# Optimization experiments

Hardware: AMD Instinct MI355X
Metric: run time of the kernel (lower is better)

## Reference

```python
import jax, jax.numpy as jnp
import numpy as np
import math

B, N, C_IN = 4, 512, 32
K = 3            # Chebyshev order -> K+1 polynomial terms
H = 4            # attention heads
OUT_PER_HEAD = 64
ACT_OUT = OUT_PER_HEAD * H  # concat_heads=True


def _prelu(x, a):
    return jnp.where(x >= 0, x, a * x)


def setup_inputs() -> dict:
    key = jax.random.key(0)
    ks = jax.random.split(key, 10)
    stdv = 1.0 / math.sqrt(ACT_OUT)
    inp = {
        "X_real": jax.random.normal(ks[0], (B, N, C_IN), jnp.float32),
        "X_imag": jax.random.normal(ks[1], (B, N, C_IN), jnp.float32),
        "L_real": jax.random.normal(ks[2], (B, K + 1, N, N), jnp.float32),
        "L_imag": jax.random.normal(ks[3], (B, K + 1, N, N), jnp.float32),
        # Chebyshev complex weights, uniform(-stdv, stdv) as in torch init
        "weight_real": jax.random.uniform(ks[4], (K + 1, C_IN, ACT_OUT), jnp.float32, -stdv, stdv),
        "weight_imag": jax.random.uniform(ks[5], (K + 1, C_IN, ACT_OUT), jnp.float32, -stdv, stdv),
        # CVLinear(2*C_IN -> H) complex weight/bias
        "attn_w_real": jax.random.normal(ks[6], (2 * C_IN, H), jnp.float32) * 0.1,
        "attn_w_imag": jax.random.normal(ks[7], (2 * C_IN, H), jnp.float32) * 0.1,
        "attn_b_real": jnp.zeros((H,), jnp.float32),
        "attn_b_imag": jnp.zeros((H,), jnp.float32),
        # CPReLU slopes (PReLU applied to real/imag parts independently)
        "prelu_a_real": jnp.float32(0.25),
        "prelu_a_imag": jnp.float32(0.25),
        "bias_real": jnp.zeros((1, ACT_OUT), jnp.float32),
        "bias_imag": jnp.zeros((1, ACT_OUT), jnp.float32),
    }
    return inp


def reference(X_real, X_imag, L_real, L_imag, weight_real, weight_imag,
              attn_w_real, attn_w_imag, attn_b_real, attn_b_imag,
              prelu_a_real, prelu_a_imag, bias_real, bias_imag):
    C = X_real.shape[-1]
    K1 = weight_real.shape[0]
    # --- attention scores: complex linear on concat([X_i, X_j]) ---
    # split the 2C weight into the X_i half and the X_j half (same math,
    # avoids materializing the B*N*N*2C pairwise concat tensor)
    W1r, W2r = attn_w_real[:C], attn_w_real[C:]
    W1i, W2i = attn_w_imag[:C], attn_w_imag[C:]
    si_re = X_real @ W1r - X_imag @ W1i   # (B,N,H)
    si_im = X_real @ W1i + X_imag @ W1r
    sj_re = X_real @ W2r - X_imag @ W2i
    sj_im = X_real @ W2i + X_imag @ W2r
    # scores[b,i,j,h]
    sc_re = si_re[:, :, None, :] + sj_re[:, None, :, :] + attn_b_real
    sc_im = si_im[:, :, None, :] + sj_im[:, None, :, :] + attn_b_imag
    # CPReLU: PReLU on real/imag independently
    sc_re = _prelu(sc_re, prelu_a_real)
    sc_im = _prelu(sc_im, prelu_a_imag)
    # adjacency mask from |L_real| summed over the K+1 polynomial terms
    mask = (jnp.abs(L_real).sum(axis=1) > 1e-9)[..., None]  # (B,N,N,1)
    NEG = jnp.float32(-1e9)
    re_m = jnp.where(mask, sc_re, NEG)
    im_m = jnp.where(mask, sc_im, NEG)
    attn = jax.nn.softmax(re_m * re_m + im_m * im_m, axis=2)  # softmax over j, (B,N,N,H)
    # --- complex Chebyshev propagation: (L*attn) @ X, per k, per head ---
    lre_xr = jnp.einsum('bknj,bnjh,bjc->bknch', L_real, attn, X_real)
    lim_xi = jnp.einsum('bknj,bnjh,bjc->bknch', L_imag, attn, X_imag)
    lre_xi = jnp.einsum('bknj,bnjh,bjc->bknch', L_real, attn, X_imag)
    lim_xr = jnp.einsum('bknj,bnjh,bjc->bknch', L_imag, attn, X_real)
    LXr = lre_xr - lim_xi
    LXi = lre_xi + lim_xr
    # per-head complex weights: (K+1, C, P, H), out index = p*H + h
    Wr = weight_real.reshape(K1, C, OUT_PER_HEAD, H)
    Wi = weight_imag.reshape(K1, C, OUT_PER_HEAD, H)
    Yre = jnp.einsum('bknch,kcph->bnph', LXr, Wr) - jnp.einsum('bknch,kcph->bnph', LXi, Wi)
    Yim = jnp.einsum('bknch,kcph->bnph', LXr, Wi) + jnp.einsum('bknch,kcph->bnph', LXi, Wr)
    Bsz, Nn = X_real.shape[:2]
    out_re = Yre.reshape(Bsz, Nn, -1) + bias_real
    out_im = Yim.reshape(Bsz, Nn, -1) + bias_imag
    return (out_re, out_im)
```

## Files before the change

### kernel.cpp

```cpp
#include <hip/hip_runtime.h>
#include <hip/hip_bf16.h>

#define BB 4
#define NN 512
#define CC 32
#define KK 4
#define HH 4
#define AOUT 256

#define WS_SI_F   0
#define WS_SII_F  (BB*NN*HH)
#define WS_SJR_F  (2*BB*NN*HH)
#define WS_SJI_F  (3*BB*NN*HH)
#define XT_BASE   131072
#define LX_BASE   393216
#define BRE_BASE  (393216 + 2048*4096)
#define BIM_BASE  (BRE_BASE + 131072)

typedef __attribute__((ext_vector_type(8))) short bf16x8;
typedef __attribute__((ext_vector_type(4))) float f32x4;

__device__ __forceinline__ ushort f2bfu(float f){
    union { __hip_bfloat16 h; ushort u; } cv;
    cv.h = __float2bfloat16(f);
    return cv.u;
}
__device__ __forceinline__ short f2bfs(float f){ return (short)f2bfu(f); }
__device__ __forceinline__ float bfu2f(unsigned int u){ return __uint_as_float(u << 16); }

__global__ __launch_bounds__(256) void prep_kernel(
    const float* __restrict__ Xr, const float* __restrict__ Xi,
    const float* __restrict__ AWr, const float* __restrict__ AWi,
    const float* __restrict__ Wr, const float* __restrict__ Wi,
    float* __restrict__ ws, char* __restrict__ wsB)
{
    const int blk = blockIdx.x;
    const int t = threadIdx.x;

    if (blk < 32) {
        const int row = blk*64 + (t >> 2);
        const int q = t & 3;
        const float* xr = Xr + (size_t)row*CC + q*8;
        const float* xi = Xi + (size_t)row*CC + q*8;
        float4 xr4[2], xi4[2];
        xr4[0] = *(const float4*)xr;  xr4[1] = *(const float4*)(xr + 4);
        xi4[0] = *(const float4*)xi;  xi4[1] = *(const float4*)(xi + 4);

        float sir[HH] = {0,0,0,0}, sii[HH] = {0,0,0,0};
        float sjr[HH] = {0,0,0,0}, sji[HH] = {0,0,0,0};
        #pragma unroll
        for (int e = 0; e < 8; ++e) {
            float xrc = ((const float*)&xr4[e>>2])[e & 3];
            float xic = ((const float*)&xi4[e>>2])[e & 3];
            int c = q*8 + e;
            float4 w1r = *(const float4*)(AWr + c*HH);
            float4 w1i = *(const float4*)(AWi + c*HH);
            float4 w2r = *(const float4*)(AWr + (CC + c)*HH);
            float4 w2i = *(const float4*)(AWi + (CC + c)*HH);
            #pragma unroll
            for (int h = 0; h < HH; ++h) {
                float r1 = ((const float*)&w1r)[h], i1 = ((const float*)&w1i)[h];
                float r2 = ((const float*)&w2r)[h], i2 = ((const float*)&w2i)[h];
                sir[h] = fmaf(xrc, r1, fmaf(-xic, i1, sir[h]));
                sii[h] = fmaf(xrc, i1, fmaf( xic, r1, sii[h]));
                sjr[h] = fmaf(xrc, r2, fmaf(-xic, i2, sjr[h]));
                sji[h] = fmaf(xrc, i2, fmaf( xic, r2, sji[h]));
            }
        }
        float A[HH], Bv[HH];
        #pragma unroll
        for (int h = 0; h < HH; ++h) {
            float sendA = (q & 1) ? sir[h] : sii[h];
            float keepA = (q & 1) ? sii[h] : sir[h];
            A[h] = keepA + __shfl_xor(sendA, 1);
            float sendB = (q & 1) ? sjr[h] : sji[h];
            float keepB = (q & 1) ? sji[h] : sjr[h];
            Bv[h] = keepB + __shfl_xor(sendB, 1);
        }
        float tot[HH];
        #pragma unroll
        for (int h = 0; h < HH; ++h) {
            float send = (q & 2) ? A[h] : Bv[h];
            float keep = (q & 2) ? Bv[h] : A[h];
            tot[h] = keep + __shfl_xor(send, 2);
        }
        float4 v = make_float4(tot[0], tot[1], tot[2], tot[3]);
        *(float4*)(ws + (size_t)q*(BB*NN*HH) + (size_t)row*HH) = v;
    } else if (blk < 64) {
        int bid = (blk - 32)*4 + (t >> 6);
        int part = bid >> 6, b = (bid >> 4) & 3, jb = bid & 15;
        const float* X = part ? Xi : Xr;
        int lane = t & 63;
        int c = lane & 31, jh = lane >> 5;

        unsigned int w[8];
        #pragma unroll
        for (int qq = 0; qq < 8; ++qq) {
            int ji = jh*16 + qq*2;
            float f0 = X[((size_t)b*NN + jb*32 + ji  )*CC + c];
            float f1 = X[((size_t)b*NN + jb*32 + ji+1)*CC + c];
            w[qq] = (unsigned int)f2bfu(f0) | ((unsigned int)f2bfu(f1) << 16);
        }
        char* tile = wsB + XT_BASE + (((size_t)(part*4 + b)*16 + jb) * 2048);
        uint4* dst = (uint4*)(tile + c*64 + jh*32);
        dst[0] = make_uint4(w[0], w[1], w[2], w[3]);
        dst[1] = make_uint4(w[4], w[5], w[6], w[7]);
    } else {
        int idx = (blk - 64)*256 + t;
        int l  = idx & 63;
        int s  = (idx >> 6) & 7;
        int Nt = (idx >> 9) & 3;
        int h  = idx >> 11;
        int p = Nt*16 + (l & 15), o = p*4 + h;
        int e8 = (l >> 4) * 8;
        unsigned int re_w[4], im_w[4];
        #pragma unroll
        for (int qq = 0; qq < 4; ++qq) {
            unsigned int rw = 0, iw = 0;
            #pragma unroll
            for (int half = 0; half < 2; ++half) {
                int kpos = s*32 + e8 + qq*2 + half;
                int ri = kpos >> 7, kk = (kpos >> 5) & 3, c = kpos & 31;
                float wr = Wr[(size_t)(kk*CC + c)*AOUT + o];
                float wi = Wi[(size_t)(kk*CC + c)*AOUT + o];
                unsigned int vre = f2bfu(ri ? -wi : wr);
                unsigned int vim = f2bfu(ri ?  wr : wi);
                rw |= vre << (16*half);
                iw |= vim << (16*half);
            }
            re_w[qq] = rw; im_w[qq] = iw;
        }
        size_t fo = ((size_t)((h*4 + Nt)*8 + s))*1024 + (size_t)l*16;
        *(uint4*)(wsB + BRE_BASE + fo) = make_uint4(re_w[0], re_w[1], re_w[2], re_w[3]);
        *(uint4*)(wsB + BIM_BASE + fo) = make_uint4(im_w[0], im_w[1], im_w[2], im_w[3]);
    }
}

__global__ __launch_bounds__(128) void cheb_main_kernel(
    const float* __restrict__ Lr_g, const float* __restrict__ Li_g,
    const float* __restrict__ abr, const float* __restrict__ abi,
    const float* __restrict__ par, const float* __restrict__ pai,
    const float* __restrict__ ws, char* __restrict__ wsB)
{
    __shared__ ushort Lf[8][528];
    __shared__ float awf[HH][520];
    __shared__ float wredm[2][HH];
    __shared__ float wreds[2][HH];

    const int bn = blockIdx.x;
    const int b = bn >> 9;
    const int n = bn & (NN - 1);
    const int t = threadIdx.x;
    const int l = t & 63;
    const int w = t >> 6;
    const int jw = 4*t;

    const float4 si_r4 = *(const float4*)(ws + WS_SI_F  + bn*HH);
    const float4 si_i4 = *(const float4*)(ws + WS_SII_F + bn*HH);
    float4 sjr[4], sji[4];
    #pragma unroll
    for (int e = 0; e < 4; ++e) {
        sjr[e] = *(const float4*)(ws + WS_SJR_F + ((size_t)b*NN + jw + e)*HH);
        sji[e] = *(const float4*)(ws + WS_SJI_F + ((size_t)b*NN + jw + e)*HH);
    }
    const float a_r = par[0], a_i = pai[0];

    float am4[4] = {0.f,0.f,0.f,0.f};
    #pragma unroll
    for (int it = 0; it < 8; ++it) {
        const float* src = (it & 4) ? Li_g : Lr_g;
        size_t goff = (((size_t)b*KK + (it & 3))*NN + n)*NN + jw;
        float4 v = *(const float4*)(src + goff);
        if (it < 4) {
            am4[0] += fabsf(v.x); am4[1] += fabsf(v.y);
            am4[2] += fabsf(v.z); am4[3] += fabsf(v.w);
        }
        ushort4 u;
        u.x = f2bfu(v.x); u.y = f2bfu(v.y); u.z = f2bfu(v.z); u.w = f2bfu(v.w);
        *(ushort4*)&Lf[it][jw] = u;
    }

    float sir[HH], sii[HH];
    #pragma unroll
    for (int h = 0; h < HH; ++h) {
        sir[h] = ((const float*)&si_r4)[h] + abr[h];
        sii[h] = ((const float*)&si_i4)[h] + abi[h];
    }
    float v[4][HH];
    float pmax[HH] = {-INFINITY, -INFINITY, -INFINITY, -INFINITY};
    #pragma unroll
    for (int e = 0; e < 4; ++e) {
        bool msk = am4[e] > 1e-9f;
        const float* sjrp = (const float*)&sjr[e];
        const float* sjip = (const float*)&sji[e];
        #pragma unroll
        for (int h = 0; h < HH; ++h) {
            float sr = sir[h] + sjrp[h];
            sr = sr >= 0.f ? sr : a_r * sr;
            float sv = sii[h] + sjip[h];
            sv = sv >= 0.f ? sv : a_i * sv;
            float val;
            if (msk) val = sr*sr + sv*sv;
            else { const float NEG = -1e9f; val = NEG*NEG + NEG*NEG; }
            v[e][h] = val;
            pmax[h] = fmaxf(pmax[h], val);
        }
    }
    #pragma unroll
    for (int h = 0; h < HH; ++h) {
        #pragma unroll
        for (int off = 32; off > 0; off >>= 1)
            pmax[h] = fmaxf(pmax[h], __shfl_xor(pmax[h], off));
    }
    if (l == 0) { wredm[w][0]=pmax[0]; wredm[w][1]=pmax[1]; wredm[w][2]=pmax[2]; wredm[w][3]=pmax[3]; }
    __syncthreads();

    float hm[HH];
    #pragma unroll
    for (int h = 0; h < HH; ++h) hm[h] = fmaxf(wredm[0][h], wredm[1][h]);

    float psum[HH];
    #pragma unroll
    for (int h = 0; h < HH; ++h) {
        float4 ev;
        ev.x = __expf(v[0][h] - hm[h]);
        ev.y = __expf(v[1][h] - hm[h]);
        ev.z = __expf(v[2][h] - hm[h]);
        ev.w = __expf(v[3][h] - hm[h]);
        *(float4*)&awf[h][jw] = ev;
        psum[h] = (ev.x + ev.y) + (ev.z + ev.w);
    }
    #pragma unroll
    for (int h = 0; h < HH; ++h) {
        #pragma unroll
        for (int off = 32; off > 0; off >>= 1)
            psum[h] += __shfl_xor(psum[h], off);
    }
    if (l == 0) { wreds[w][0]=psum[0]; wreds[w][1]=psum[1]; wreds[w][2]=psum[2]; wreds[w][3]=psum[3]; }
    __syncthreads();

    float inv[HH];
    #pragma unroll
    for (int h = 0; h < HH; ++h) inv[h] = 1.0f / (wreds[0][h] + wreds[1][h]);

    const int r_a = l & 15;
    const int jg  = l >> 4;
    const int k_a = r_a >> 2, h_a = r_a & 3;

    f32x4 acc[8];
    #pragma unroll
    for (int a = 0; a < 8; ++a) acc[a] = (f32x4){0.f,0.f,0.f,0.f};

    const char* xtR = wsB + XT_BASE + ((size_t)(0*4 + b)*16 + w*8)*2048;
    const char* xtI = wsB + XT_BASE + ((size_t)(4   + b)*16 + w*8)*2048;
    const int bofs = (l & 15)*64 + jg*16;

#define LOAD_STEP(s, BR0,BR1,BI0,BI1, LR8,LI8, AW0,AW1) do {                  \
        const int j0_ = w*256 + (s)*32 + jg*8;                                \
        BR0 = *(const bf16x8*)(xtR + (s)*2048 +        bofs);                 \
        BR1 = *(const bf16x8*)(xtR + (s)*2048 + 1024 + bofs);                 \
        BI0 = *(const bf16x8*)(xtI + (s)*2048 +        bofs);                 \
        BI1 = *(const bf16x8*)(xtI + (s)*2048 + 1024 + bofs);                 \
        LR8 = *(const bf16x8*)&Lf[k_a][j0_];                                  \
        LI8 = *(const bf16x8*)&Lf[4 + k_a][j0_];                              \
        AW0 = *(const float4*)&awf[h_a][j0_];                                 \
        AW1 = *(const float4*)&awf[h_a][j0_ + 4];                             \
    } while (0)

#define COMP_STEP(BR0,BR1,BI0,BI1, LR8,LI8, AW0,AW1) do {                     \
        float aww_[8];                                                        \
        *(float4*)&aww_[0] = AW0; *(float4*)&aww_[4] = AW1;                   \
        bf16x8 Ar_, Ai_;                                                      \
        _Pragma("unroll")                                                     \
        for (int e_ = 0; e_ < 8; ++e_) {                                      \
            Ar_[e_] = f2bfs(bfu2f((ushort)LR8[e_]) * aww_[e_]);               \
            Ai_[e_] = f2bfs(bfu2f((ushort)LI8[e_]) * aww_[e_]);               \
        }                                                                     \
        acc[0] = __builtin_amdgcn_mfma_f32_16x16x32_bf16(Ar_, BR0, acc[0],0,0,0); \
        acc[1] = __builtin_amdgcn_mfma_f32_16x16x32_bf16(Ar_, BR1, acc[1],0,0,0); \
        acc[2] = __builtin_amdgcn_mfma_f32_16x16x32_bf16(Ai_, BI0, acc[2],0,0,0); \
        acc[3] = __builtin_amdgcn_mfma_f32_16x16x32_bf16(Ai_, BI1, acc[3],0,0,0); \
        acc[4] = __builtin_amdgcn_mfma_f32_16x16x32_bf16(Ar_, BI0, acc[4],0,0,0); \
        acc[5] = __builtin_amdgcn_mfma_f32_16x16x32_bf16(Ar_, BI1, acc[5],0,0,0); \
        acc[6] = __builtin_amdgcn_mfma_f32_16x16x32_bf16(Ai_, BR0, acc[6],0,0,0); \
        acc[7] = __builtin_amdgcn_mfma_f32_16x16x32_bf16(Ai_, BR1, acc[7],0,0,0); \
    } while (0)

    {
        bf16x8 pBr0,pBr1,pBi0,pBi1,pLr,pLi; float4 pA0,pA1;
        bf16x8 qBr0,qBr1,qBi0,qBi1,qLr,qLi; float4 qA0,qA1;
        LOAD_STEP(0, pBr0,pBr1,pBi0,pBi1, pLr,pLi, pA0,pA1);
        LOAD_STEP(1, qBr0,qBr1,qBi0,qBi1, qLr,qLi, qA0,qA1);
        COMP_STEP(pBr0,pBr1,pBi0,pBi1, pLr,pLi, pA0,pA1);
        LOAD_STEP(2, pBr0,pBr1,pBi0,pBi1, pLr,pLi, pA0,pA1);
        COMP_STEP(qBr0,qBr1,qBi0,qBi1, qLr,qLi, qA0,qA1);
        LOAD_STEP(3, qBr0,qBr1,qBi0,qBi1, qLr,qLi, qA0,qA1);
        COMP_STEP(pBr0,pBr1,pBi0,pBi1, pLr,pLi, pA0,pA1);
        LOAD_STEP(4, pBr0,pBr1,pBi0,pBi1, pLr,pLi, pA0,pA1);
        COMP_STEP(qBr0,qBr1,qBi0,qBi1, qLr,qLi, qA0,qA1);
        LOAD_STEP(5, qBr0,qBr1,qBi0,qBi1, qLr,qLi, qA0,qA1);
        COMP_STEP(pBr0,pBr1,pBi0,pBi1, pLr,pLi, pA0,pA1);
        LOAD_STEP(6, pBr0,pBr1,pBi0,pBi1, pLr,pLi, pA0,pA1);
        COMP_STEP(qBr0,qBr1,qBi0,qBi1, qLr,qLi, qA0,qA1);
        LOAD_STEP(7, qBr0,qBr1,qBi0,qBi1, qLr,qLi, qA0,qA1);
        COMP_STEP(pBr0,pBr1,pBi0,pBi1, pLr,pLi, pA0,pA1);
        COMP_STEP(qBr0,qBr1,qBi0,qBi1, qLr,qLi, qA0,qA1);
    }
#undef LOAD_STEP
#undef COMP_STEP

    const int kk = l >> 4, lc = l & 15;
    char* lxp = wsB + LX_BASE + (size_t)bn*4096 + (size_t)w*2048;
    #pragma unroll
    for (int ct = 0; ct < 2; ++ct) {
        const int c = ct*16 + lc;
        #pragma unroll
        for (int r = 0; r < 4; ++r) {
            float iv = inv[r];
            float vr = (acc[0+ct][r] - acc[2+ct][r]) * iv;
            float vi = (acc[4+ct][r] + acc[6+ct][r]) * iv;
            *(ushort*)(lxp + r*512 +       kk*64 + c*2) = f2bfu(vr);
            *(ushort*)(lxp + r*512 + 256 + kk*64 + c*2) = f2bfu(vi);
        }
    }
}

__global__ __launch_bounds__(256) void out_gemm_kernel(
    const char* __restrict__ wsB,
    const float* __restrict__ bsr, const float* __restrict__ bsi,
    float* __restrict__ out)
{
    const int Mtile = blockIdx.x >> 2;
    const int Nt    = blockIdx.x & 3;
    const int t = threadIdx.x, l = t & 63, h = t >> 6;

    const char* abase0 = wsB + LX_BASE + ((size_t)(Mtile*16 + (l & 15)))*4096
                         + h*512 + (l >> 4)*16;
    const char* abase1 = abase0 + 2048;
    f32x4 are = (f32x4){0.f,0.f,0.f,0.f};
    f32x4 aim = (f32x4){0.f,0.f,0.f,0.f};
    const size_t fbase = ((size_t)((h*4 + Nt)*8))*1024 + (size_t)l*16;
    const char* bre = wsB + BRE_BASE + fbase;
    const char* bim = wsB + BIM_BASE + fbase;
    #pragma unroll
    for (int s = 0; s < 8; ++s) {
        bf16x8 Af0 = *(const bf16x8*)(abase0 + s*64);
        bf16x8 Af1 = *(const bf16x8*)(abase1 + s*64);
        bf16x8 Br  = *(const bf16x8*)(bre + s*1024);
        bf16x8 Bi  = *(const bf16x8*)(bim + s*1024);
        are = __builtin_amdgcn_mfma_f32_16x16x32_bf16(Af0, Br, are, 0, 0, 0);
        are = __builtin_amdgcn_mfma_f32_16x16x32_bf16(Af1, Br, are, 0, 0, 0);
        aim = __builtin_amdgcn_mfma_f32_16x16x32_bf16(Af0, Bi, aim, 0, 0, 0);
        aim = __builtin_amdgcn_mfma_f32_16x16x32_bf16(Af1, Bi, aim, 0, 0, 0);
    }
    const int p = Nt*16 + (l & 15), o = p*4 + h;
    const float vbr = bsr[o], vbi = bsi[o];
    #pragma unroll
    for (int r = 0; r < 4; ++r) {
        int bn = Mtile*16 + (l >> 4)*4 + r;
        out[(size_t)bn*AOUT + o] = are[r] + vbr;
        out[(size_t)BB*NN*AOUT + (size_t)bn*AOUT + o] = aim[r] + vbi;
    }
}

extern "C" void kernel_launch(void* const* d_in, const int* in_sizes, int n_in,
                              void* d_out, int out_size, void* d_ws, size_t ws_size,
                              hipStream_t stream)
{
    const float* Xr  = (const float*)d_in[0];
    const float* Xi  = (const float*)d_in[1];
    const float* Lr  = (const float*)d_in[2];
    const float* Li  = (const float*)d_in[3];
    const float* Wr  = (const float*)d_in[4];
    const float* Wi  = (const float*)d_in[5];
    const float* AWr = (const float*)d_in[6];
    const float* AWi = (const float*)d_in[7];
    const float* abr = (const float*)d_in[8];
    const float* abi = (const float*)d_in[9];
    const float* par = (const float*)d_in[10];
    const float* pai = (const float*)d_in[11];
    const float* bsr = (const float*)d_in[12];
    const float* bsi = (const float*)d_in[13];
    float* ws  = (float*)d_ws;
    char*  wsB = (char*)d_ws;
    float* out = (float*)d_out;

    hipLaunchKernelGGL(prep_kernel, dim3(96), dim3(256), 0, stream,
                       Xr, Xi, AWr, AWi, Wr, Wi, ws, wsB);
    hipLaunchKernelGGL(cheb_main_kernel, dim3(BB*NN), dim3(128), 0, stream,
                       Lr, Li, abr, abi, par, pai, ws, wsB);
    hipLaunchKernelGGL(out_gemm_kernel, dim3(512), dim3(256), 0, stream,
                       wsB, bsr, bsi, out);
}
```

Baseline: 38.32 us.

## Reduce split-K partials in LDS before storing LX, halve output GEMM loads

The propagation kernel previously had two waves each write their own partial LX slice, which the output GEMM then summed with extra MFMAs. Now wave 1 writes its accumulators to shared memory, wave 0 adds them and writes one combined LX row, halving the LX workspace and the A-operand loads and MFMAs in the output GEMM. It also wraps the MFMA burst in s_setprio to favour the issuing wave. The cost is an extra pair of barriers and LDS traffic, and wave 0 alone runs the epilogue.

```diff
diff --git a/kernel.cpp b/kernel.cpp
--- a/kernel.cpp
+++ b/kernel.cpp
@@ -14,8 +14,8 @@
 #define WS_SJI_F  (3*BB*NN*HH)
 #define XT_BASE   131072
 #define LX_BASE   393216
-#define BRE_BASE  (393216 + 2048*4096)
-#define BIM_BASE  (BRE_BASE + 131072)
+#define BRE_BASE  4587520
+#define BIM_BASE  4718592
 
 typedef __attribute__((ext_vector_type(8))) short bf16x8;
 typedef __attribute__((ext_vector_type(4))) float f32x4;
@@ -276,6 +276,7 @@
             Ar_[e_] = f2bfs(bfu2f((ushort)LR8[e_]) * aww_[e_]);               \
             Ai_[e_] = f2bfs(bfu2f((ushort)LI8[e_]) * aww_[e_]);               \
         }                                                                     \
+        __builtin_amdgcn_s_setprio(1);                                        \
         acc[0] = __builtin_amdgcn_mfma_f32_16x16x32_bf16(Ar_, BR0, acc[0],0,0,0); \
         acc[1] = __builtin_amdgcn_mfma_f32_16x16x32_bf16(Ar_, BR1, acc[1],0,0,0); \
         acc[2] = __builtin_amdgcn_mfma_f32_16x16x32_bf16(Ai_, BI0, acc[2],0,0,0); \
@@ -284,6 +285,7 @@
         acc[5] = __builtin_amdgcn_mfma_f32_16x16x32_bf16(Ar_, BI1, acc[5],0,0,0); \
         acc[6] = __builtin_amdgcn_mfma_f32_16x16x32_bf16(Ai_, BR0, acc[6],0,0,0); \
         acc[7] = __builtin_amdgcn_mfma_f32_16x16x32_bf16(Ai_, BR1, acc[7],0,0,0); \
+        __builtin_amdgcn_s_setprio(0);                                        \
     } while (0)
 
     {
@@ -309,18 +311,36 @@
 #undef LOAD_STEP
 #undef COMP_STEP
 
-    const int kk = l >> 4, lc = l & 15;
-    char* lxp = wsB + LX_BASE + (size_t)bn*4096 + (size_t)w*2048;
-    #pragma unroll
-    for (int ct = 0; ct < 2; ++ct) {
-        const int c = ct*16 + lc;
-        #pragma unroll
-        for (int r = 0; r < 4; ++r) {
-            float iv = inv[r];
-            float vr = (acc[0+ct][r] - acc[2+ct][r]) * iv;
-            float vi = (acc[4+ct][r] + acc[6+ct][r]) * iv;
-            *(ushort*)(lxp + r*512 +       kk*64 + c*2) = f2bfu(vr);
-            *(ushort*)(lxp + r*512 + 256 + kk*64 + c*2) = f2bfu(vi);
+    __syncthreads();
+
+    float* pbuf = &awf[0][0];
+    if (w == 1) {
+        #pragma unroll
+        for (int a = 0; a < 8; ++a)
+            #pragma unroll
+            for (int r = 0; r < 4; ++r)
+                pbuf[(a*4 + r)*64 + l] = acc[a][r];
+    }
+    __syncthreads();
+    if (w == 0) {
+        const int kk = l >> 4, lc = l & 15;
+        #pragma unroll
+        for (int a = 0; a < 8; ++a)
+            #pragma unroll
+            for (int r = 0; r < 4; ++r)
+                acc[a][r] += pbuf[(a*4 + r)*64 + l];
+        char* lxp = wsB + LX_BASE + (size_t)bn*2048;
+        #pragma unroll
+        for (int ct = 0; ct < 2; ++ct) {
+            const int c = ct*16 + lc;
+            #pragma unroll
+            for (int r = 0; r < 4; ++r) {
+                float iv = inv[r];
+                float vr = (acc[0+ct][r] - acc[2+ct][r]) * iv;
+                float vi = (acc[4+ct][r] + acc[6+ct][r]) * iv;
+                *(ushort*)(lxp + r*512 +       kk*64 + c*2) = f2bfu(vr);
+                *(ushort*)(lxp + r*512 + 256 + kk*64 + c*2) = f2bfu(vi);
+            }
         }
     }
 }
@@ -334,9 +354,8 @@
     const int Nt    = blockIdx.x & 3;
     const int t = threadIdx.x, l = t & 63, h = t >> 6;
 
-    const char* abase0 = wsB + LX_BASE + ((size_t)(Mtile*16 + (l & 15)))*4096
-                         + h*512 + (l >> 4)*16;
-    const char* abase1 = abase0 + 2048;
+    const char* abase = wsB + LX_BASE + ((size_t)(Mtile*16 + (l & 15)))*2048
+                        + h*512 + (l >> 4)*16;
     f32x4 are = (f32x4){0.f,0.f,0.f,0.f};
     f32x4 aim = (f32x4){0.f,0.f,0.f,0.f};
     const size_t fbase = ((size_t)((h*4 + Nt)*8))*1024 + (size_t)l*16;
@@ -344,14 +363,11 @@
     const char* bim = wsB + BIM_BASE + fbase;
     #pragma unroll
     for (int s = 0; s < 8; ++s) {
-        bf16x8 Af0 = *(const bf16x8*)(abase0 + s*64);
-        bf16x8 Af1 = *(const bf16x8*)(abase1 + s*64);
-        bf16x8 Br  = *(const bf16x8*)(bre + s*1024);
-        bf16x8 Bi  = *(const bf16x8*)(bim + s*1024);
-        are = __builtin_amdgcn_mfma_f32_16x16x32_bf16(Af0, Br, are, 0, 0, 0);
-        are = __builtin_amdgcn_mfma_f32_16x16x32_bf16(Af1, Br, are, 0, 0, 0);
-        aim = __builtin_amdgcn_mfma_f32_16x16x32_bf16(Af0, Bi, aim, 0, 0, 0);
-        aim = __builtin_amdgcn_mfma_f32_16x16x32_bf16(Af1, Bi, aim, 0, 0, 0);
+        bf16x8 Af = *(const bf16x8*)(abase + s*64);
+        bf16x8 Br = *(const bf16x8*)(bre + s*1024);
+        bf16x8 Bi = *(const bf16x8*)(bim + s*1024);
+        are = __builtin_amdgcn_mfma_f32_16x16x32_bf16(Af, Br, are, 0, 0, 0);
+        aim = __builtin_amdgcn_mfma_f32_16x16x32_bf16(Af, Bi, aim, 0, 0, 0);
     }
     const int p = Nt*16 + (l & 15), o = p*4 + h;
     const float vbr = bsr[o], vbi = bsi[o];
```

Result: faster. 34.08 us (-11.1%).
